# Kernel tuning notes

Measured on AMD Instinct MI355X. Metric: run time of the kernel, lower is better.

The kernel has to match this reference:

```python
import jax, jax.numpy as jnp
import numpy as np

N_NODES = 100000
N_EDGES = 1600000
IN_CH = 128
EDGE_CH = 32
HEADS = 4
OUT_CH = 32
NEG_SLOPE = 0.2
EPS = 1e-16  # matches torch_geometric softmax denominator epsilon


def setup_inputs() -> dict:
    key = jax.random.key(0)
    ks = jax.random.split(key, 8)
    x = jax.random.normal(ks[0], (N_NODES, IN_CH), dtype=jnp.float32)
    edge_attr = jax.random.normal(ks[1], (N_EDGES, EDGE_CH), dtype=jnp.float32)
    # glorot-ish scaled params
    Wl = jax.random.normal(ks[2], (HEADS * OUT_CH, IN_CH), dtype=jnp.float32) * (1.0 / np.sqrt(IN_CH))
    We = jax.random.normal(ks[3], (HEADS * OUT_CH, EDGE_CH), dtype=jnp.float32) * (1.0 / np.sqrt(EDGE_CH))
    att_l = jax.random.normal(ks[4], (1, HEADS, OUT_CH), dtype=jnp.float32) * 0.1
    att_r = jax.random.normal(ks[5], (1, HEADS, OUT_CH), dtype=jnp.float32) * 0.1
    att_e = jax.random.normal(ks[6], (1, HEADS, OUT_CH), dtype=jnp.float32) * 0.1
    bias = jnp.zeros((HEADS * OUT_CH,), dtype=jnp.float32)
    edge_index = jax.random.randint(ks[7], (2, N_EDGES), 0, N_NODES, dtype=jnp.int32)
    return {"x": x, "edge_attr": edge_attr, "Wl": Wl, "We": We,
            "att_l": att_l, "att_r": att_r, "att_e": att_e,
            "bias": bias, "edge_index": edge_index}


def reference(x, edge_attr, Wl, We, att_l, att_r, att_e, bias, edge_index):
    N = x.shape[0]
    H, C = att_l.shape[1], att_l.shape[2]
    # shared lin_l == lin_r projection  [N, H, C]
    xl = (x @ Wl.T).reshape(N, H, C)
    alpha_l = (xl * att_l).sum(-1)          # [N, H] source term
    alpha_r = (xl * att_r).sum(-1)          # [N, H] target term
    # edge feature projection            [E, H, C]
    e = (edge_attr @ We.T).reshape(-1, H, C)
    alpha_e = (e * att_e).sum(-1)           # [E, H]
    src, dst = edge_index[0], edge_index[1]
    # per-edge attention logits
    alpha = alpha_l[src] + alpha_r[dst] + alpha_e        # [E, H]
    alpha = jax.nn.leaky_relu(alpha, NEG_SLOPE)
    # segment softmax over incoming edges of each target node
    amax = jax.ops.segment_max(alpha, dst, num_segments=N)   # [N, H]
    ex = jnp.exp(alpha - amax[dst])
    denom = jax.ops.segment_sum(ex, dst, num_segments=N)     # [N, H]
    alpha_n = ex / (denom[dst] + EPS)                        # [E, H]
    # weighted scatter-add aggregation of source features
    msg = xl[src] * alpha_n[:, :, None]                      # [E, H, C]
    out = jax.ops.segment_sum(msg, dst, num_segments=N)      # [N, H, C]
    out = out.reshape(N, H * C) + bias                       # concat heads
    return out
```

## Files before the change

kernel.cpp:

```cpp
#include <hip/hip_runtime.h>
#include <hip/hip_fp16.h>

#define NN 100000
#define NE 1600000
#define NB 391
#define NEG 0.2f

#define OFF_XLB   ((size_t)0)
#define OFF_AL    ((size_t)6400000)
#define OFF_AR    ((size_t)6800000)
#define OFF_WE    ((size_t)7200000)
#define OFF_REC   ((size_t)7200128)
#define OFF_TMP   ((size_t)13600128)
#define OFF_BSUM  (OFF_TMP + 110000)
#define OFF_DEG   ((size_t)15200128)
#define OFF_ROW   ((size_t)15300128)

__device__ __forceinline__ unsigned short f2bf(float f) {
    unsigned u = __float_as_uint(f);
    u += 0x7fffu + ((u >> 16) & 1u);
    return (unsigned short)(u >> 16);
}
__device__ __forceinline__ float bf2f(unsigned short v) {
    return __uint_as_float((unsigned)v << 16);
}

__global__ void k_prep_zero(const float* __restrict__ We, const float* __restrict__ att_e,
                            float* __restrict__ we, int* __restrict__ deg) {
    int i = blockIdx.x * 256 + threadIdx.x;
    if (i < NN) deg[i] = 0;
    if (blockIdx.x == 0 && threadIdx.x < 128) {
        int t = threadIdx.x, h = t >> 5, k = t & 31;
        float s = 0.f;
        for (int c = 0; c < 32; ++c)
            s += att_e[h * 32 + c] * We[(size_t)(h * 32 + c) * 32 + k];
        we[t] = s;
    }
}

__global__ void k_hist(const int* __restrict__ ei, int* __restrict__ deg) {
    int e = blockIdx.x * 256 + threadIdx.x;
    atomicAdd(&deg[ei[NE + e]], 1);
}

__global__ __launch_bounds__(256, 2) void k_node(
        const float* __restrict__ x, const float* __restrict__ Wl,
        const float* __restrict__ attl, const float* __restrict__ attr_,
        unsigned short* __restrict__ xlb, float* __restrict__ al, float* __restrict__ ar) {
    __shared__ float wT[128 * 128];
    __shared__ float xT[128 * 32];
    int t = threadIdx.x;
    int og = t & 31, ng = t >> 5;
    int nb = blockIdx.x * 32;

    {
        int o = t & 127, q = t >> 7;
        #pragma unroll
        for (int chunk = 0; chunk < 16; ++chunk) {
            int k0 = chunk * 8 + q * 4;
            float4 w = *(const float4*)&Wl[(size_t)o * 128 + k0];
            wT[(k0 + 0) * 128 + o] = w.x;
            wT[(k0 + 1) * 128 + o] = w.y;
            wT[(k0 + 2) * 128 + o] = w.z;
            wT[(k0 + 3) * 128 + o] = w.w;
        }
    }
    {
        int n = t & 31, q = t >> 5;
        #pragma unroll
        for (int chunk = 0; chunk < 4; ++chunk) {
            int k0 = chunk * 32 + q * 4;
            float4 v = *(const float4*)&x[(size_t)(nb + n) * 128 + k0];
            xT[(k0 + 0) * 32 + n] = v.x;
            xT[(k0 + 1) * 32 + n] = v.y;
            xT[(k0 + 2) * 32 + n] = v.z;
            xT[(k0 + 3) * 32 + n] = v.w;
        }
    }
    float4 attl4 = *(const float4*)&attl[og * 4];
    float4 attr4 = *(const float4*)&attr_[og * 4];
    __syncthreads();

    float4 a0 = make_float4(0,0,0,0), a1 = a0, a2 = a0, a3 = a0;
    #pragma unroll 8
    for (int k = 0; k < 128; ++k) {
        float4 w  = *(const float4*)&wT[k * 128 + og * 4];
        float4 xv = *(const float4*)&xT[k * 32  + ng * 4];
        a0.x += w.x * xv.x; a0.y += w.y * xv.x; a0.z += w.z * xv.x; a0.w += w.w * xv.x;
        a1.x += w.x * xv.y; a1.y += w.y * xv.y; a1.z += w.z * xv.y; a1.w += w.w * xv.y;
        a2.x += w.x * xv.z; a2.y += w.y * xv.z; a2.z += w.z * xv.z; a2.w += w.w * xv.z;
        a3.x += w.x * xv.w; a3.y += w.y * xv.w; a3.z += w.z * xv.w; a3.w += w.w * xv.w;
    }

    float4 accs[4] = {a0, a1, a2, a3};
    #pragma unroll
    for (int j = 0; j < 4; ++j) {
        int node = nb + ng * 4 + j;
        ushort4 pk;
        pk.x = f2bf(accs[j].x); pk.y = f2bf(accs[j].y);
        pk.z = f2bf(accs[j].z); pk.w = f2bf(accs[j].w);
        *(ushort4*)&xlb[(size_t)node * 128 + og * 4] = pk;
        float pl = accs[j].x * attl4.x + accs[j].y * attl4.y +
                   accs[j].z * attl4.z + accs[j].w * attl4.w;
        float pr = accs[j].x * attr4.x + accs[j].y * attr4.y +
                   accs[j].z * attr4.z + accs[j].w * attr4.w;
        #pragma unroll
        for (int off = 1; off <= 4; off <<= 1) {
            pl += __shfl_xor(pl, off);
            pr += __shfl_xor(pr, off);
        }
        if ((og & 7) == 0) {
            al[(size_t)node * 4 + (og >> 3)] = pl;
            ar[(size_t)node * 4 + (og >> 3)] = pr;
        }
    }
}

__global__ void k_scan_block(const int* __restrict__ deg, int* __restrict__ row_tmp,
                             int* __restrict__ bsum) {
    __shared__ int sh[256];
    int t = threadIdx.x, i = blockIdx.x * 256 + t;
    int d = (i < NN) ? deg[i] : 0;
    int v = d;
    sh[t] = v; __syncthreads();
    for (int off = 1; off < 256; off <<= 1) {
        int add = (t >= off) ? sh[t - off] : 0;
        __syncthreads();
        v += add; sh[t] = v; __syncthreads();
    }
    if (i < NN) row_tmp[i] = v - d;
    if (t == 255) bsum[blockIdx.x] = v;
}

__global__ void k_scan_top(int* __restrict__ bsum) {
    __shared__ int sh[512];
    int t = threadIdx.x;
    int d = (t < NB) ? bsum[t] : 0;
    int v = d;
    sh[t] = v; __syncthreads();
    for (int off = 1; off < 512; off <<= 1) {
        int add = (t >= off) ? sh[t - off] : 0;
        __syncthreads();
        v += add; sh[t] = v; __syncthreads();
    }
    if (t < NB) bsum[t] = v - d;
}

__global__ void k_scan_add(const int* __restrict__ row_tmp, const int* __restrict__ bsum,
                           int* __restrict__ row, int* __restrict__ cursor) {
    int i = blockIdx.x * 256 + threadIdx.x;
    if (i < NN) {
        int v = row_tmp[i] + bsum[i >> 8];
        row[i] = v;
        cursor[i] = v;
    }
    if (i == 0) row[NN] = NE;
}

__global__ __launch_bounds__(256) void k_edge(
        const float* __restrict__ eattr, const int* __restrict__ ei,
        const float* __restrict__ al, const float* __restrict__ ar,
        const float* __restrict__ we, int* __restrict__ cursor,
        float4* __restrict__ rec) {
    __shared__ __align__(16) float wsh[128];
    if (threadIdx.x < 128) wsh[threadIdx.x] = we[threadIdx.x];
    __syncthreads();
    int e = blockIdx.x * 256 + threadIdx.x;
    int src = ei[e], dst = ei[NE + e];
    const float4* ea = (const float4*)(eattr + (size_t)e * 32);
    float a[4] = {0.f, 0.f, 0.f, 0.f};
    #pragma unroll
    for (int r = 0; r < 8; ++r) {
        float4 v = ea[r];
        #pragma unroll
        for (int h = 0; h < 4; ++h) {
            float4 w = *(const float4*)&wsh[h * 32 + r * 4];
            a[h] += v.x * w.x + v.y * w.y + v.z * w.z + v.w * w.w;
        }
    }
    float4 ls = *(const float4*)&al[(size_t)src * 4];
    float4 rs = *(const float4*)&ar[(size_t)dst * 4];
    a[0] += ls.x + rs.x; a[1] += ls.y + rs.y;
    a[2] += ls.z + rs.z; a[3] += ls.w + rs.w;
    #pragma unroll
    for (int h = 0; h < 4; ++h) {
        float v = a[h] > 0.f ? a[h] : NEG * a[h];
        a[h] = __expf(fminf(v, 60.f));
    }
    __half2 h01 = __floats2half2_rn(a[0], a[1]);
    __half2 h23 = __floats2half2_rn(a[2], a[3]);
    int slot = atomicAdd(&cursor[dst], 1);
    float4 r;
    r.x = __uint_as_float((unsigned)src);
    r.y = *reinterpret_cast<float*>(&h01);
    r.z = *reinterpret_cast<float*>(&h23);
    r.w = 0.f;
    rec[slot] = r;
}

__device__ __forceinline__ float pick_p(const float4& r, int h) {
    __half2 h01 = *reinterpret_cast<const __half2*>(&r.y);
    __half2 h23 = *reinterpret_cast<const __half2*>(&r.z);
    float2 p01 = __half22float2(h01);
    float2 p23 = __half22float2(h23);
    float lo = (h & 2) ? p23.x : p01.x;
    float hi = (h & 2) ? p23.y : p01.y;
    return (h & 1) ? hi : lo;
}

__global__ __launch_bounds__(128) void k_out(
        const int* __restrict__ row, const float4* __restrict__ rec,
        const unsigned short* __restrict__ xlb,
        const float* __restrict__ bias, float* __restrict__ out) {
    int n = blockIdx.x;
    int t = threadIdx.x, h = t >> 5;
    int s0 = row[n], s1 = row[n + 1];

    float l0 = 0.f, l1 = 0.f, l2 = 0.f, l3 = 0.f;
    float O0 = 0.f, O1 = 0.f, O2 = 0.f, O3 = 0.f;
    int s = s0;
    for (; s + 4 <= s1; s += 4) {
        float4 r0 = rec[s + 0], r1 = rec[s + 1];
        float4 r2 = rec[s + 2], r3 = rec[s + 3];
        int src0 = (int)__float_as_uint(r0.x), src1 = (int)__float_as_uint(r1.x);
        int src2 = (int)__float_as_uint(r2.x), src3 = (int)__float_as_uint(r3.x);
        unsigned short v0 = xlb[(size_t)src0 * 128 + t];
        unsigned short v1 = xlb[(size_t)src1 * 128 + t];
        unsigned short v2 = xlb[(size_t)src2 * 128 + t];
        unsigned short v3 = xlb[(size_t)src3 * 128 + t];
        float p0 = pick_p(r0, h), p1 = pick_p(r1, h);
        float p2 = pick_p(r2, h), p3 = pick_p(r3, h);
        l0 += p0; l1 += p1; l2 += p2; l3 += p3;
        O0 += p0 * bf2f(v0); O1 += p1 * bf2f(v1);
        O2 += p2 * bf2f(v2); O3 += p3 * bf2f(v3);
    }
    for (; s < s1; ++s) {
        float4 r = rec[s];
        int srcn = (int)__float_as_uint(r.x);
        float p = pick_p(r, h);
        l0 += p;
        O0 += p * bf2f(xlb[(size_t)srcn * 128 + t]);
    }
    float l = (l0 + l1) + (l2 + l3);
    float O = (O0 + O1) + (O2 + O3);
    out[(size_t)n * 128 + t] = O / (l + 1e-16f) + bias[t];
}

extern "C" void kernel_launch(void* const* d_in, const int* in_sizes, int n_in,
                              void* d_out, int out_size, void* d_ws, size_t ws_size,
                              hipStream_t stream) {
    const float* x     = (const float*)d_in[0];
    const float* eattr = (const float*)d_in[1];
    const float* Wl    = (const float*)d_in[2];
    const float* We    = (const float*)d_in[3];
    const float* att_l = (const float*)d_in[4];
    const float* att_r = (const float*)d_in[5];
    const float* att_e = (const float*)d_in[6];
    const float* bias  = (const float*)d_in[7];
    const int*   ei    = (const int*)d_in[8];
    float* out = (float*)d_out;

    float* ws = (float*)d_ws;
    unsigned short* xlb = (unsigned short*)(ws + OFF_XLB);
    float* al      = ws + OFF_AL;
    float* ar      = ws + OFF_AR;
    float* we      = ws + OFF_WE;
    float4* rec    = (float4*)(ws + OFF_REC);
    int*   row_tmp = (int*)(ws + OFF_TMP);
    int*   bsum    = (int*)(ws + OFF_BSUM);
    int*   deg     = (int*)(ws + OFF_DEG);
    int*   rowp    = (int*)(ws + OFF_ROW);

    k_prep_zero<<<NB, 256, 0, stream>>>(We, att_e, we, deg);
    k_hist<<<NE / 256, 256, 0, stream>>>(ei, deg);
    k_node<<<NN / 32, 256, 0, stream>>>(x, Wl, att_l, att_r, xlb, al, ar);
    k_scan_block<<<NB, 256, 0, stream>>>(deg, row_tmp, bsum);
    k_scan_top<<<1, 512, 0, stream>>>(bsum);
    k_scan_add<<<NB, 256, 0, stream>>>(row_tmp, bsum, rowp, deg);
    k_edge<<<NE / 256, 256, 0, stream>>>(eattr, ei, al, ar, we, deg, rec);
    k_out<<<NN, 128, 0, stream>>>(rowp, rec, xlb, bias, out);
}
```

Before: 651.3 us.

## Split edge pass into alpha compute and two-pass range-partitioned scatter

Fuses the degree histogram into a new per-edge alpha kernel that writes packed half-precision probabilities to an edge-ordered buffer. A separate scatter kernel then places src and probabilities into CSR order as structure-of-arrays, run in two passes over destination halves so each pass's atomics and scattered writes touch a smaller address range. The record shrinks from a 16-byte float4 to 12 bytes split across two arrays. The cost is extra passes over edge_index and the alpha buffer, plus an extra kernel launch.

Result: no change. 660.2 us (+1.4%).

```diff
diff --git a/kernel.cpp b/kernel.cpp
--- a/kernel.cpp
+++ b/kernel.cpp
@@ -5,14 +5,17 @@
 #define NE 1600000
 #define NB 391
 #define NEG 0.2f
+#define NHALF 50000
 
 #define OFF_XLB   ((size_t)0)
 #define OFF_AL    ((size_t)6400000)
 #define OFF_AR    ((size_t)6800000)
 #define OFF_WE    ((size_t)7200000)
-#define OFF_REC   ((size_t)7200128)
-#define OFF_TMP   ((size_t)13600128)
-#define OFF_BSUM  (OFF_TMP + 110000)
+#define OFF_RECP  ((size_t)7200128)
+#define OFF_RECS  ((size_t)10400128)
+#define OFF_PAL   ((size_t)12000128)
+#define OFF_TMP   OFF_RECP
+#define OFF_BSUM  (OFF_RECP + 110000)
 #define OFF_DEG   ((size_t)15200128)
 #define OFF_ROW   ((size_t)15300128)
 
@@ -36,11 +39,6 @@
             s += att_e[h * 32 + c] * We[(size_t)(h * 32 + c) * 32 + k];
         we[t] = s;
     }
-}
-
-__global__ void k_hist(const int* __restrict__ ei, int* __restrict__ deg) {
-    int e = blockIdx.x * 256 + threadIdx.x;
-    atomicAdd(&deg[ei[NE + e]], 1);
 }
 
 __global__ __launch_bounds__(256, 2) void k_node(
@@ -116,6 +114,45 @@
     }
 }
 
+__global__ __launch_bounds__(256) void k_alpha(
+        const float* __restrict__ eattr, const int* __restrict__ ei,
+        const float* __restrict__ al, const float* __restrict__ ar,
+        const float* __restrict__ we, int* __restrict__ deg,
+        float2* __restrict__ palpha) {
+    __shared__ __align__(16) float wsh[128];
+    if (threadIdx.x < 128) wsh[threadIdx.x] = we[threadIdx.x];
+    __syncthreads();
+    int e = blockIdx.x * 256 + threadIdx.x;
+    int src = ei[e], dst = ei[NE + e];
+    const float4* ea = (const float4*)(eattr + (size_t)e * 32);
+    float a[4] = {0.f, 0.f, 0.f, 0.f};
+    #pragma unroll
+    for (int r = 0; r < 8; ++r) {
+        float4 v = ea[r];
+        #pragma unroll
+        for (int h = 0; h < 4; ++h) {
+            float4 w = *(const float4*)&wsh[h * 32 + r * 4];
+            a[h] += v.x * w.x + v.y * w.y + v.z * w.z + v.w * w.w;
+        }
+    }
+    float4 ls = *(const float4*)&al[(size_t)src * 4];
+    float4 rs = *(const float4*)&ar[(size_t)dst * 4];
+    a[0] += ls.x + rs.x; a[1] += ls.y + rs.y;
+    a[2] += ls.z + rs.z; a[3] += ls.w + rs.w;
+    #pragma unroll
+    for (int h = 0; h < 4; ++h) {
+        float v = a[h] > 0.f ? a[h] : NEG * a[h];
+        a[h] = __expf(fminf(v, 60.f));
+    }
+    __half2 h01 = __floats2half2_rn(a[0], a[1]);
+    __half2 h23 = __floats2half2_rn(a[2], a[3]);
+    float2 p;
+    p.x = *reinterpret_cast<float*>(&h01);
+    p.y = *reinterpret_cast<float*>(&h23);
+    palpha[e] = p;
+    atomicAdd(&deg[dst], 1);
+}
+
 __global__ void k_scan_block(const int* __restrict__ deg, int* __restrict__ row_tmp,
                              int* __restrict__ bsum) {
     __shared__ int sh[256];
@@ -157,50 +194,24 @@
     if (i == 0) row[NN] = NE;
 }
 
-__global__ __launch_bounds__(256) void k_edge(
-        const float* __restrict__ eattr, const int* __restrict__ ei,
-        const float* __restrict__ al, const float* __restrict__ ar,
-        const float* __restrict__ we, int* __restrict__ cursor,
-        float4* __restrict__ rec) {
-    __shared__ __align__(16) float wsh[128];
-    if (threadIdx.x < 128) wsh[threadIdx.x] = we[threadIdx.x];
-    __syncthreads();
+__global__ __launch_bounds__(256) void k_scat(
+        const int* __restrict__ ei, const float2* __restrict__ palpha,
+        int* __restrict__ cursor, int* __restrict__ rec_src,
+        float2* __restrict__ rec_p, int lo, int hi) {
     int e = blockIdx.x * 256 + threadIdx.x;
-    int src = ei[e], dst = ei[NE + e];
-    const float4* ea = (const float4*)(eattr + (size_t)e * 32);
-    float a[4] = {0.f, 0.f, 0.f, 0.f};
-    #pragma unroll
-    for (int r = 0; r < 8; ++r) {
-        float4 v = ea[r];
-        #pragma unroll
-        for (int h = 0; h < 4; ++h) {
-            float4 w = *(const float4*)&wsh[h * 32 + r * 4];
-            a[h] += v.x * w.x + v.y * w.y + v.z * w.z + v.w * w.w;
-        }
-    }
-    float4 ls = *(const float4*)&al[(size_t)src * 4];
-    float4 rs = *(const float4*)&ar[(size_t)dst * 4];
-    a[0] += ls.x + rs.x; a[1] += ls.y + rs.y;
-    a[2] += ls.z + rs.z; a[3] += ls.w + rs.w;
-    #pragma unroll
-    for (int h = 0; h < 4; ++h) {
-        float v = a[h] > 0.f ? a[h] : NEG * a[h];
-        a[h] = __expf(fminf(v, 60.f));
-    }
-    __half2 h01 = __floats2half2_rn(a[0], a[1]);
-    __half2 h23 = __floats2half2_rn(a[2], a[3]);
-    int slot = atomicAdd(&cursor[dst], 1);
-    float4 r;
-    r.x = __uint_as_float((unsigned)src);
-    r.y = *reinterpret_cast<float*>(&h01);
-    r.z = *reinterpret_cast<float*>(&h23);
-    r.w = 0.f;
-    rec[slot] = r;
-}
-
-__device__ __forceinline__ float pick_p(const float4& r, int h) {
-    __half2 h01 = *reinterpret_cast<const __half2*>(&r.y);
-    __half2 h23 = *reinterpret_cast<const __half2*>(&r.z);
+    int dst = ei[NE + e];
+    int src = ei[e];
+    float2 p = palpha[e];
+    if (dst >= lo && dst < hi) {
+        int slot = atomicAdd(&cursor[dst], 1);
+        rec_src[slot] = src;
+        rec_p[slot] = p;
+    }
+}
+
+__device__ __forceinline__ float pick_p(float2 q, int h) {
+    __half2 h01 = *reinterpret_cast<const __half2*>(&q.x);
+    __half2 h23 = *reinterpret_cast<const __half2*>(&q.y);
     float2 p01 = __half22float2(h01);
     float2 p23 = __half22float2(h23);
     float lo = (h & 2) ? p23.x : p01.x;
@@ -209,8 +220,8 @@
 }
 
 __global__ __launch_bounds__(128) void k_out(
-        const int* __restrict__ row, const float4* __restrict__ rec,
-        const unsigned short* __restrict__ xlb,
+        const int* __restrict__ row, const int* __restrict__ rec_src,
+        const float2* __restrict__ rec_p, const unsigned short* __restrict__ xlb,
         const float* __restrict__ bias, float* __restrict__ out) {
     int n = blockIdx.x;
     int t = threadIdx.x, h = t >> 5;
@@ -220,24 +231,23 @@
     float O0 = 0.f, O1 = 0.f, O2 = 0.f, O3 = 0.f;
     int s = s0;
     for (; s + 4 <= s1; s += 4) {
-        float4 r0 = rec[s + 0], r1 = rec[s + 1];
-        float4 r2 = rec[s + 2], r3 = rec[s + 3];
-        int src0 = (int)__float_as_uint(r0.x), src1 = (int)__float_as_uint(r1.x);
-        int src2 = (int)__float_as_uint(r2.x), src3 = (int)__float_as_uint(r3.x);
+        int src0 = rec_src[s + 0], src1 = rec_src[s + 1];
+        int src2 = rec_src[s + 2], src3 = rec_src[s + 3];
+        float2 q0 = rec_p[s + 0], q1 = rec_p[s + 1];
+        float2 q2 = rec_p[s + 2], q3 = rec_p[s + 3];
         unsigned short v0 = xlb[(size_t)src0 * 128 + t];
         unsigned short v1 = xlb[(size_t)src1 * 128 + t];
         unsigned short v2 = xlb[(size_t)src2 * 128 + t];
         unsigned short v3 = xlb[(size_t)src3 * 128 + t];
-        float p0 = pick_p(r0, h), p1 = pick_p(r1, h);
-        float p2 = pick_p(r2, h), p3 = pick_p(r3, h);
+        float p0 = pick_p(q0, h), p1 = pick_p(q1, h);
+        float p2 = pick_p(q2, h), p3 = pick_p(q3, h);
         l0 += p0; l1 += p1; l2 += p2; l3 += p3;
         O0 += p0 * bf2f(v0); O1 += p1 * bf2f(v1);
         O2 += p2 * bf2f(v2); O3 += p3 * bf2f(v3);
     }
     for (; s < s1; ++s) {
-        float4 r = rec[s];
-        int srcn = (int)__float_as_uint(r.x);
-        float p = pick_p(r, h);
+        int srcn = rec_src[s];
+        float p = pick_p(rec_p[s], h);
         l0 += p;
         O0 += p * bf2f(xlb[(size_t)srcn * 128 + t]);
     }
@@ -262,21 +272,24 @@
 
     float* ws = (float*)d_ws;
     unsigned short* xlb = (unsigned short*)(ws + OFF_XLB);
-    float* al      = ws + OFF_AL;
-    float* ar      = ws + OFF_AR;
-    float* we      = ws + OFF_WE;
-    float4* rec    = (float4*)(ws + OFF_REC);
-    int*   row_tmp = (int*)(ws + OFF_TMP);
-    int*   bsum    = (int*)(ws + OFF_BSUM);
-    int*   deg     = (int*)(ws + OFF_DEG);
-    int*   rowp    = (int*)(ws + OFF_ROW);
+    float*  al      = ws + OFF_AL;
+    float*  ar      = ws + OFF_AR;
+    float*  we      = ws + OFF_WE;
+    float2* rec_p   = (float2*)(ws + OFF_RECP);
+    int*    rec_src = (int*)(ws + OFF_RECS);
+    float2* palpha  = (float2*)(ws + OFF_PAL);
+    int*    row_tmp = (int*)(ws + OFF_TMP);
+    int*    bsum    = (int*)(ws + OFF_BSUM);
+    int*    deg     = (int*)(ws + OFF_DEG);
+    int*    rowp    = (int*)(ws + OFF_ROW);
 
     k_prep_zero<<<NB, 256, 0, stream>>>(We, att_e, we, deg);
-    k_hist<<<NE / 256, 256, 0, stream>>>(ei, deg);
     k_node<<<NN / 32, 256, 0, stream>>>(x, Wl, att_l, att_r, xlb, al, ar);
+    k_alpha<<<NE / 256, 256, 0, stream>>>(eattr, ei, al, ar, we, deg, palpha);
     k_scan_block<<<NB, 256, 0, stream>>>(deg, row_tmp, bsum);
     k_scan_top<<<1, 512, 0, stream>>>(bsum);
     k_scan_add<<<NB, 256, 0, stream>>>(row_tmp, bsum, rowp, deg);
-    k_edge<<<NE / 256, 256, 0, stream>>>(eattr, ei, al, ar, we, deg, rec);
-    k_out<<<NN, 128, 0, stream>>>(rowp, rec, xlb, bias, out);
-}
+    k_scat<<<NE / 256, 256, 0, stream>>>(ei, palpha, deg, rec_src, rec_p, 0, NHALF);
+    k_scat<<<NE / 256, 256, 0, stream>>>(ei, palpha, deg, rec_src, rec_p, NHALF, NN);
+    k_out<<<NN, 128, 0, stream>>>(rowp, rec_src, rec_p, xlb, bias, out);
+}
```
